# Kernel optimization log

Measured on AMD Instinct MI355X. Metric: run time of the kernel, lower is better.

## Reference

```python
import jax, jax.numpy as jnp
import numpy as np

B, C, H, W = 4, 96, 56, 56
K = 9          # kernel_size * dilation, dilation=1 so DenseDilated is identity
GROUPS = 4     # gcn_lib BasicConv uses groups=4 for the edge MLP 1x1 conv
EPS_BN = 1e-5
EPS_NORM = 1e-12


def _bn(x, p):
    # eval-mode BatchNorm2d: p = [gamma, beta, running_mean, running_var], each [C]
    g, b, m, v = p
    inv = g / jnp.sqrt(v + EPS_BN)
    sh = (1, -1) + (1,) * (x.ndim - 2)
    return x * inv.reshape(sh) + (b - m * inv).reshape(sh)


def _bn_params(k, c):
    k1, k2, k3, k4 = jax.random.split(k, 4)
    return jnp.stack([
        1.0 + 0.1 * jax.random.normal(k1, (c,)),
        0.1 * jax.random.normal(k2, (c,)),
        0.1 * jax.random.normal(k3, (c,)),
        jax.random.uniform(k4, (c,), minval=0.5, maxval=1.5),
    ])


def setup_inputs() -> dict:
    key = jax.random.key(0)
    ks = jax.random.split(key, 8)
    C2 = 2 * C
    return {
        "x": jax.random.normal(ks[0], (B, C, H, W), jnp.float32),
        "fc1_w": jax.random.normal(ks[1], (C, C), jnp.float32) / np.float32(np.sqrt(C)),
        "fc1_b": jnp.zeros((C,), jnp.float32),
        "bn1": _bn_params(ks[2], C),
        "gc_w": jax.random.normal(ks[3], (GROUPS, C2 // GROUPS, C2 // GROUPS), jnp.float32) / np.float32(np.sqrt(C2 // GROUPS)),
        "gc_b": jnp.zeros((C2,), jnp.float32),
        "bng": _bn_params(ks[4], C2),
        "fc2_w": jax.random.normal(ks[5], (C, C2), jnp.float32) / np.float32(np.sqrt(C2)),
        "fc2_b": jnp.zeros((C,), jnp.float32),
        "bn2": _bn_params(ks[6], C),
    }


def reference(x, fc1_w, fc1_b, bn1, gc_w, gc_b, bng, fc2_w, fc2_b, bn2):
    res = x
    # fc1: 1x1 conv + BN
    x = _bn(jnp.einsum('oc,bchw->bohw', fc1_w, x) + fc1_b[None, :, None, None], bn1)
    b, c, h, w = x.shape
    n = h * w
    xf = x.reshape(b, c, n)                       # [B,C,N] node features

    # --- dynamic kNN graph (torch.no_grad in original) ---
    xg = jax.lax.stop_gradient(xf)
    norm = jnp.sqrt(jnp.sum(xg * xg, axis=1, keepdims=True))
    xn = xg / jnp.maximum(norm, EPS_NORM)         # F.normalize along channels
    xt = xn.transpose(0, 2, 1)                    # [B,N,C]
    sq = jnp.sum(xt * xt, axis=-1)                # [B,N]
    neg_dist = 2.0 * jnp.einsum('bnc,bmc->bnm', xt, xt) - sq[:, :, None] - sq[:, None, :]
    _, nn_idx = jax.lax.top_k(neg_dist, K)        # [B,N,K] nearest neighbors

    # --- EdgeConv: gather, edge MLP (grouped 1x1 conv + BN + ReLU), max-aggregate ---
    x_j = jax.vmap(lambda f, idx: f[:, idx])(xf, nn_idx)   # [B,C,N,K]
    x_i = xf[:, :, :, None]                                 # [B,C,N,1]
    feat = jnp.concatenate([jnp.broadcast_to(x_i, x_j.shape), x_j - x_i], axis=1)  # [B,2C,N,K]
    c2 = 2 * c
    fg = feat.reshape(b, GROUPS, c2 // GROUPS, n, K)
    y = jnp.einsum('goc,bgcnk->bgonk', gc_w, fg).reshape(b, c2, n, K)
    y = y + gc_b[None, :, None, None]
    y = jax.nn.relu(_bn(y, bng))
    y = jnp.max(y, axis=-1)                       # max over K neighbors -> [B,2C,N]
    y = y.reshape(b, c2, h, w)

    # fc2: 1x1 conv + BN, residual
    y = _bn(jnp.einsum('oc,bchw->bohw', fc2_w, y) + fc2_b[None, :, None, None], bn2)
    return y + res
```

## Files before the change

kernel.cpp:

```cpp
#include <hip/hip_runtime.h>
#include <cstdint>
#include <cstddef>
#include <math.h>

#define BN_   4
#define CC    96
#define C2    192
#define NN    3136
#define KNN   9
#define TILE  64
#define PT    8
#define FJR   580
#define WTS   100

typedef __attribute__((ext_vector_type(8))) __bf16 bf16x8;
typedef __attribute__((ext_vector_type(4))) float f32x4;

__device__ __forceinline__ unsigned short f2bf(float f) {
  unsigned int u = __float_as_uint(f);
  unsigned int r = u + 0x7fffu + ((u >> 16) & 1u);
  return (unsigned short)(r >> 16);
}
__device__ __forceinline__ float bf2f(unsigned short h) {
  return __uint_as_float(((unsigned int)h) << 16);
}
__device__ __forceinline__ unsigned int fmono(float f) {
  unsigned int s = __float_as_uint(f);
  return s ^ ((unsigned int)((int)s >> 31) | 0x80000000u);
}

__device__ __forceinline__ void topk_ins(uint64_t key, uint64_t (&bk)[KNN]) {
  if (key > bk[KNN - 1]) {
    #pragma unroll
    for (int j = KNN - 1; j >= 1; --j) {
      bool aj   = bk[j]     > key;
      bool ajm1 = bk[j - 1] > key;
      bk[j] = aj ? bk[j] : (ajm1 ? key : bk[j - 1]);
    }
    bk[0] = (bk[0] > key) ? bk[0] : key;
  }
}

__global__ __launch_bounds__(256) void k_fc1(const float* __restrict__ x,
                                             const float* __restrict__ w,
                                             const float* __restrict__ bias,
                                             const float* __restrict__ bn,
                                             float* __restrict__ y1t,
                                             unsigned short* __restrict__ xh,
                                             unsigned short* __restrict__ xl,
                                             float* __restrict__ sq) {
  __shared__ float xs[CC * 64];
  __shared__ float wT[CC * WTS];
  __shared__ __align__(16) float ys[64 * CC];
  const int b = blockIdx.y, n0 = blockIdx.x * 64;
  const int t = threadIdx.x;
  for (int i = t; i < CC * 64; i += 256) {
    int c = i >> 6, nn = i & 63;
    xs[i] = x[((size_t)b * CC + c) * NN + n0 + nn];
  }
  for (int i = t; i < CC * CC; i += 256) {
    int o = i / CC, c = i % CC;
    wT[c * WTS + o] = w[i];
  }
  __syncthreads();
  const int nn = t & 63;
  const int og = __builtin_amdgcn_readfirstlane(t >> 6);
  float acc[24];
  #pragma unroll
  for (int i = 0; i < 24; ++i) acc[i] = 0.f;
  for (int c = 0; c < CC; ++c) {
    float xv = xs[c * 64 + nn];
    const float* wp = &wT[c * WTS + og * 24];
    float4 w0 = *(const float4*)(wp);
    float4 w1 = *(const float4*)(wp + 4);
    float4 w2 = *(const float4*)(wp + 8);
    float4 w3 = *(const float4*)(wp + 12);
    float4 w4 = *(const float4*)(wp + 16);
    float4 w5 = *(const float4*)(wp + 20);
    const float wv[24] = {w0.x, w0.y, w0.z, w0.w, w1.x, w1.y, w1.z, w1.w,
                          w2.x, w2.y, w2.z, w2.w, w3.x, w3.y, w3.z, w3.w,
                          w4.x, w4.y, w4.z, w4.w, w5.x, w5.y, w5.z, w5.w};
    #pragma unroll
    for (int oi = 0; oi < 24; ++oi) acc[oi] = fmaf(wv[oi], xv, acc[oi]);
  }
  #pragma unroll
  for (int oi = 0; oi < 24; ++oi) {
    int o = og * 24 + oi;
    float g = bn[o], be = bn[CC + o], mn = bn[2 * CC + o], vr = bn[3 * CC + o];
    float inv = g / sqrtf(vr + 1e-5f);
    float v = fmaf(acc[oi] + bias[o], inv, be - mn * inv);
    y1t[((size_t)b * NN + n0 + nn) * CC + o] = v;
    ys[nn * CC + o] = v;
  }
  __syncthreads();

  if (t < 64) {
    const size_t p = (size_t)b * NN + n0 + t;
    const float* row = &ys[t * CC];
    float s = 0.f;
    for (int c = 0; c < CC; c += 4) {
      float4 v = *(const float4*)(row + c);
      s += v.x * v.x; s += v.y * v.y; s += v.z * v.z; s += v.w * v.w;
    }
    float inv = 1.f / fmaxf(sqrtf(s), 1e-12f);
    float sqs = 0.f;
    unsigned short* hrow = xh + p * CC;
    unsigned short* lrow = xl + p * CC;
    for (int c = 0; c < CC; c += 4) {
      float4 v4 = *(const float4*)(row + c);
      float v0 = v4.x * inv, v1 = v4.y * inv, v2 = v4.z * inv, v3 = v4.w * inv;
      sqs += v0 * v0; sqs += v1 * v1; sqs += v2 * v2; sqs += v3 * v3;
      unsigned short h0 = f2bf(v0), h1 = f2bf(v1), h2 = f2bf(v2), h3 = f2bf(v3);
      float l0 = v0 - bf2f(h0), l1 = v1 - bf2f(h1), l2 = v2 - bf2f(h2), l3 = v3 - bf2f(h3);
      uint2 hv, lv;
      hv.x = (unsigned int)h0 | ((unsigned int)h1 << 16);
      hv.y = (unsigned int)h2 | ((unsigned int)h3 << 16);
      lv.x = (unsigned int)f2bf(l0) | ((unsigned int)f2bf(l1) << 16);
      lv.y = (unsigned int)f2bf(l2) | ((unsigned int)f2bf(l3) << 16);
      *(uint2*)&hrow[c] = hv;
      *(uint2*)&lrow[c] = lv;
    }
    sq[p] = sqs;
  }
}

__global__ __launch_bounds__(256) void k_dist(const unsigned short* __restrict__ xh,
                                              const unsigned short* __restrict__ xl,
                                              const float* __restrict__ sq,
                                              uint64_t* __restrict__ cand_k) {
  __shared__ __align__(16) unsigned short sB[2 * 64 * 104];
  __shared__ __align__(16) float sqm[TILE];
  unsigned short* BsH = sB;
  unsigned short* BsL = sB + 64 * 104;

  const int rt = blockIdx.x, chunk = blockIdx.y, b = blockIdx.z;
  const int nch = gridDim.y;
  const int r0 = rt * TILE;
  const int t = threadIdx.x;
  const int lane = t & 63, w = t >> 6;
  const int m16 = lane & 15, quad = lane >> 4;
  const int mt0 = (49 * chunk) / nch, mt1 = (49 * (chunk + 1)) / nch;

  const int gr = r0 + w * 16 + m16;
  bf16x8 ah[3], al[3];
  {
    const unsigned short* pH = xh + ((size_t)b * NN + gr) * CC + quad * 8;
    const unsigned short* pL = xl + ((size_t)b * NN + gr) * CC + quad * 8;
    #pragma unroll
    for (int kc = 0; kc < 3; ++kc) {
      ah[kc] = *(const bf16x8*)(pH + kc * 32);
      al[kc] = *(const bf16x8*)(pL + kc * 32);
    }
  }
  const float sr = sq[b * NN + gr];

  uint64_t bk[KNN];
  #pragma unroll
  for (int j = 0; j < KNN; ++j) bk[j] = 0ull;

  for (int mt = mt0; mt < mt1; ++mt) {
    const int m0 = mt * TILE;
    __syncthreads();
    for (int i = t; i < 64 * 12; i += 256) {
      int r = i / 12, ch = i % 12;
      const uint4* sH = (const uint4*)(xh + ((size_t)b * NN + m0 + r) * CC);
      const uint4* sL = (const uint4*)(xl + ((size_t)b * NN + m0 + r) * CC);
      *(uint4*)&BsH[r * 104 + ch * 8] = sH[ch];
      *(uint4*)&BsL[r * 104 + ch * 8] = sL[ch];
    }
    if (t < TILE) sqm[t] = sq[b * NN + m0 + t];
    __syncthreads();

    #pragma unroll
    for (int tt = 0; tt < 4; ++tt) {
      const int brow = (tt * 16 + m16) * 104 + quad * 8;
      f32x4 acc = {0.f, 0.f, 0.f, 0.f};
      #pragma unroll
      for (int kc = 0; kc < 3; ++kc) {
        bf16x8 bh = *(const bf16x8*)&BsH[brow + kc * 32];
        bf16x8 bl = *(const bf16x8*)&BsL[brow + kc * 32];
        acc = __builtin_amdgcn_mfma_f32_16x16x32_bf16(bh, ah[kc], acc, 0, 0, 0);
        acc = __builtin_amdgcn_mfma_f32_16x16x32_bf16(bl, ah[kc], acc, 0, 0, 0);
        acc = __builtin_amdgcn_mfma_f32_16x16x32_bf16(bh, al[kc], acc, 0, 0, 0);
      }
      float4 s4 = *(const float4*)&sqm[tt * 16 + quad * 4];
      const float sv[4] = {s4.x, s4.y, s4.z, s4.w};
      #pragma unroll
      for (int r = 0; r < 4; ++r) {
        float v = 2.f * acc[r] - sr - sv[r];
        int col = m0 + tt * 16 + quad * 4 + r;
        uint64_t key = ((uint64_t)fmono(v) << 32) | (unsigned int)~col;
        topk_ins(key, bk);
      }
    }
  }
  __syncthreads();

  uint64_t* sk = (uint64_t*)sB;
  #pragma unroll
  for (int j = 0; j < KNN; ++j) sk[((w * 16 + m16) * 4 + quad) * KNN + j] = bk[j];
  __syncthreads();
  if (t < TILE) {
    uint64_t fk[KNN];
    #pragma unroll
    for (int j = 0; j < KNN; ++j) fk[j] = 0ull;
    for (int qq = 0; qq < 4; ++qq)
      #pragma unroll
      for (int j = 0; j < KNN; ++j)
        topk_ins(sk[(t * 4 + qq) * KNN + j], fk);
    size_t base = (((size_t)b * nch + chunk) * NN + r0 + t) * KNN;
    #pragma unroll
    for (int j = 0; j < KNN; ++j) cand_k[base + j] = fk[j];
  }
}

__global__ __launch_bounds__(256) void k_nnmerge(const uint64_t* __restrict__ cand_k,
                                                 int* __restrict__ nn_idx, int nch) {
  __shared__ uint64_t sk[64 * 4 * KNN];
  const int t = threadIdx.x, lane = t & 63, sw = t >> 6;
  const int p = blockIdx.x * 64 + lane;
  const int b = p / NN, n = p % NN;
  const int cpw = nch >> 2;
  uint64_t fk[KNN];
  #pragma unroll
  for (int j = 0; j < KNN; ++j) fk[j] = 0ull;
  for (int ch = sw * cpw; ch < (sw + 1) * cpw; ++ch) {
    size_t base = (((size_t)b * nch + ch) * NN + n) * KNN;
    #pragma unroll
    for (int j = 0; j < KNN; ++j) topk_ins(cand_k[base + j], fk);
  }
  #pragma unroll
  for (int j = 0; j < KNN; ++j) sk[(lane * 4 + sw) * KNN + j] = fk[j];
  __syncthreads();
  if (sw == 0) {
    uint64_t gk[KNN];
    #pragma unroll
    for (int j = 0; j < KNN; ++j) gk[j] = 0ull;
    for (int q = 0; q < 4; ++q)
      #pragma unroll
      for (int j = 0; j < KNN; ++j)
        topk_ins(sk[(lane * 4 + q) * KNN + j], gk);
    #pragma unroll
    for (int j = 0; j < KNN; ++j) {
      int v = (int)(~(unsigned int)gk[j]);
      if ((unsigned)v >= (unsigned)NN) v = 0;
      nn_idx[(size_t)p * KNN + j] = v;
    }
  }
}

__global__ __launch_bounds__(256) void k_gconv(const float* __restrict__ y1t,
                                               const int* __restrict__ nn_idx,
                                               const float* __restrict__ gw,
                                               const float* __restrict__ gb,
                                               const float* __restrict__ bng,
                                               float* __restrict__ ymax) {
  __shared__ float wl[C2 * 49];
  __shared__ float xi[PT * CC];
  __shared__ __align__(16) float fj[PT * 2 * FJR];
  __shared__ int idxl[PT * KNN];
  const int t = threadIdx.x;
  const int p0 = blockIdx.x * PT;
  const int b0 = p0 / NN;

  for (int i = t; i < C2 * 48; i += 256) wl[(i / 48) * 49 + (i % 48)] = gw[i];
  if (t < PT * KNN) {
    int v = nn_idx[(size_t)p0 * KNN + t];
    idxl[t] = ((unsigned)v < (unsigned)NN) ? v : 0;
  }
  for (int i = t; i < PT * CC; i += 256) xi[i] = y1t[(size_t)p0 * CC + i];
  __syncthreads();

  for (int i = t; i < PT * KNN * CC; i += 256) {
    int pk = i / CC, c = i % CC;
    int p = pk / KNN, k = pk % KNN;
    int j = idxl[p * KNN + k];
    float v = y1t[((size_t)b0 * NN + j) * CC + c] - xi[p * CC + c];
    int h = (c >= 48) ? 1 : 0;
    fj[((p * 2 + h) * FJR) + (c - h * 48) * 12 + k] = v;
  }
  __syncthreads();

  const int p = t >> 5, l = t & 31;
  const size_t pg = p0 + p;
  float* orow = ymax + pg * C2;
  const float* xip = xi + p * CC;

  auto bnrelu = [&](int oc, float a) -> float {
    float g = bng[oc], be = bng[C2 + oc], mn = bng[2 * C2 + oc], vr = bng[3 * C2 + oc];
    float inv = g / sqrtf(vr + 1e-5f);
    return fmaxf(fmaf(a + gb[oc], inv, be - mn * inv), 0.f);
  };

  {
    const int oc0 = l, oc1 = l + 32, oc2 = l + 64;
    const int cb0 = (oc0 / 48) * 48, cb1 = (oc1 / 48) * 48, cb2 = (oc2 / 48) * 48;
    float a0 = 0.f, a1 = 0.f, a2 = 0.f;
    #pragma unroll 8
    for (int c = 0; c < 48; ++c) {
      a0 = fmaf(wl[oc0 * 49 + c], xip[cb0 + c], a0);
      a1 = fmaf(wl[oc1 * 49 + c], xip[cb1 + c], a1);
      a2 = fmaf(wl[oc2 * 49 + c], xip[cb2 + c], a2);
    }
    orow[oc0] = bnrelu(oc0, a0);
    orow[oc1] = bnrelu(oc1, a1);
    orow[oc2] = bnrelu(oc2, a2);
  }
  {
    const int half = l >> 4, lsub = l & 15;
    const int oc0 = 96 + half * 48 + lsub, oc1 = oc0 + 16, oc2 = oc0 + 32;
    const float* fbase = fj + ((size_t)p * 2 + half) * FJR;
    float acc0[KNN], acc1[KNN], acc2[KNN];
    #pragma unroll
    for (int k = 0; k < KNN; ++k) { acc0[k] = 0.f; acc1[k] = 0.f; acc2[k] = 0.f; }
    #pragma unroll 2
    for (int c = 0; c < 48; ++c) {
      float w0 = wl[oc0 * 49 + c], w1 = wl[oc1 * 49 + c], w2 = wl[oc2 * 49 + c];
      const float* fr = fbase + c * 12;
      float4 fA = *(const float4*)(fr);
      float4 fB = *(const float4*)(fr + 4);
      float f8 = fr[8];
      const float fk[KNN] = {fA.x, fA.y, fA.z, fA.w, fB.x, fB.y, fB.z, fB.w, f8};
      #pragma unroll
      for (int k = 0; k < KNN; ++k) {
        acc0[k] = fmaf(w0, fk[k], acc0[k]);
        acc1[k] = fmaf(w1, fk[k], acc1[k]);
        acc2[k] = fmaf(w2, fk[k], acc2[k]);
      }
    }
    {
      float g = bng[oc0], be = bng[C2 + oc0], mn = bng[2 * C2 + oc0], vr = bng[3 * C2 + oc0];
      float inv = g / sqrtf(vr + 1e-5f), sh = be - mn * inv, bs = gb[oc0], m = 0.f;
      #pragma unroll
      for (int k = 0; k < KNN; ++k) m = fmaxf(m, fmaxf(fmaf(acc0[k] + bs, inv, sh), 0.f));
      orow[oc0] = m;
    }
    {
      float g = bng[oc1], be = bng[C2 + oc1], mn = bng[2 * C2 + oc1], vr = bng[3 * C2 + oc1];
      float inv = g / sqrtf(vr + 1e-5f), sh = be - mn * inv, bs = gb[oc1], m = 0.f;
      #pragma unroll
      for (int k = 0; k < KNN; ++k) m = fmaxf(m, fmaxf(fmaf(acc1[k] + bs, inv, sh), 0.f));
      orow[oc1] = m;
    }
    {
      float g = bng[oc2], be = bng[C2 + oc2], mn = bng[2 * C2 + oc2], vr = bng[3 * C2 + oc2];
      float inv = g / sqrtf(vr + 1e-5f), sh = be - mn * inv, bs = gb[oc2], m = 0.f;
      #pragma unroll
      for (int k = 0; k < KNN; ++k) m = fmaxf(m, fmaxf(fmaf(acc2[k] + bs, inv, sh), 0.f));
      orow[oc2] = m;
    }
  }
}

__global__ __launch_bounds__(256) void k_fc2(const float* __restrict__ ymax,
                                             const float* __restrict__ w2,
                                             const float* __restrict__ b2,
                                             const float* __restrict__ bn2,
                                             const float* __restrict__ xin,
                                             float* __restrict__ out) {
  __shared__ float ys[64 * 193];
  __shared__ float w2T[C2 * WTS];
  const int b = blockIdx.y, n0 = blockIdx.x * 64, t = threadIdx.x;
  for (int i = t; i < 64 * C2; i += 256) {
    int nn = i / C2, c2 = i % C2;
    ys[nn * 193 + c2] = ymax[((size_t)b * NN + n0 + nn) * C2 + c2];
  }
  for (int i = t; i < CC * C2; i += 256) {
    int o = i / C2, c2 = i % C2;
    w2T[c2 * WTS + o] = w2[i];
  }
  __syncthreads();
  const int nn = t & 63;
  const int og = __builtin_amdgcn_readfirstlane(t >> 6);
  float acc[24];
  #pragma unroll
  for (int i = 0; i < 24; ++i) acc[i] = 0.f;
  const float* yrow = ys + nn * 193;
  for (int c2 = 0; c2 < C2; ++c2) {
    float yv = yrow[c2];
    const float* wp = &w2T[c2 * WTS + og * 24];
    float4 w0 = *(const float4*)(wp);
    float4 w1 = *(const float4*)(wp + 4);
    float4 w2v = *(const float4*)(wp + 8);
    float4 w3 = *(const float4*)(wp + 12);
    float4 w4 = *(const float4*)(wp + 16);
    float4 w5 = *(const float4*)(wp + 20);
    const float wv[24] = {w0.x, w0.y, w0.z, w0.w, w1.x, w1.y, w1.z, w1.w,
                          w2v.x, w2v.y, w2v.z, w2v.w, w3.x, w3.y, w3.z, w3.w,
                          w4.x, w4.y, w4.z, w4.w, w5.x, w5.y, w5.z, w5.w};
    #pragma unroll
    for (int oi = 0; oi < 24; ++oi) acc[oi] = fmaf(wv[oi], yv, acc[oi]);
  }
  #pragma unroll
  for (int oi = 0; oi < 24; ++oi) {
    int o = og * 24 + oi;
    float g = bn2[o], be = bn2[CC + o], mn = bn2[2 * CC + o], vr = bn2[3 * CC + o];
    float inv = g / sqrtf(vr + 1e-5f);
    float v = fmaf(acc[oi] + b2[o], inv, be - mn * inv);
    size_t off = ((size_t)b * CC + o) * NN + n0 + nn;
    out[off] = v + xin[off];
  }
}

extern "C" void kernel_launch(void* const* d_in, const int* in_sizes, int n_in,
                              void* d_out, int out_size, void* d_ws, size_t ws_size,
                              hipStream_t stream) {
  const float* x     = (const float*)d_in[0];
  const float* fc1_w = (const float*)d_in[1];
  const float* fc1_b = (const float*)d_in[2];
  const float* bn1   = (const float*)d_in[3];
  const float* gc_w  = (const float*)d_in[4];
  const float* gc_b  = (const float*)d_in[5];
  const float* bng   = (const float*)d_in[6];
  const float* fc2_w = (const float*)d_in[7];
  const float* fc2_b = (const float*)d_in[8];
  const float* bn2   = (const float*)d_in[9];
  float* out = (float*)d_out;

  const size_t BNC = (size_t)BN_ * NN * CC;
  float* ws = (float*)d_ws;
  float* y1t = ws;
  unsigned short* xh = (unsigned short*)(y1t + BNC);
  unsigned short* xl = xh + BNC;
  float* sq     = ws + 2 * BNC;
  float* ymax   = sq + (size_t)BN_ * NN;
  int* nnidx = (int*)(ymax + (size_t)BN_ * NN * C2);

  const size_t base_bytes =
      (2 * BNC + (size_t)BN_ * NN + (size_t)BN_ * NN * C2) * 4 +
      (size_t)BN_ * NN * KNN * 4;
  const size_t need16 = base_bytes + (size_t)BN_ * 16 * NN * KNN * 8;
  int nch;
  uint64_t* cand_k;
  if (ws_size >= need16) {
    nch = 16;
    cand_k = (uint64_t*)((char*)d_ws + base_bytes);
  } else {
    nch = 8;
    cand_k = (uint64_t*)ymax;
  }

  k_fc1<<<dim3(NN / 64, BN_), 256, 0, stream>>>(x, fc1_w, fc1_b, bn1, y1t, xh, xl, sq);
  k_dist<<<dim3(NN / TILE, nch, BN_), 256, 0, stream>>>(xh, xl, sq, cand_k);
  k_nnmerge<<<dim3((BN_ * NN) / 64), 256, 0, stream>>>(cand_k, nnidx, nch);
  k_gconv<<<dim3((BN_ * NN) / PT), 256, 0, stream>>>(y1t, nnidx, gc_w, gc_b, bng, ymax);
  k_fc2<<<dim3(NN / 64, BN_), 256, 0, stream>>>(ymax, fc2_w, fc2_b, bn2, x, out);
}
```

Baseline: 287.8 us.

## Precompute edge-conv linear map per node and gather projected features

Uses linearity of the grouped 1x1 conv: W*(x_j - x_i) = z_j - z_i, where z = W*x is computed once per node in the fc1 kernel. The x_i half of the edge MLP is also computed there and written straight to ymax. The gconv kernel becomes a light gather-subtract-BN-ReLU-max kernel, which removes the per-edge matmul work (about 9x redundant) and the large shared-memory staging. In exchange, fc1 does more compute and holds more shared memory, which may lower its occupancy. The workspace fallback logic also changes: candidates no longer alias ymax, and there is a 4-chunk fallback, since ymax is now written earlier.

```diff
diff --git a/kernel.cpp b/kernel.cpp
--- a/kernel.cpp
+++ b/kernel.cpp
@@ -10,8 +10,8 @@
 #define KNN   9
 #define TILE  64
 #define PT    8
-#define FJR   580
 #define WTS   100
+#define YSS   100
 
 typedef __attribute__((ext_vector_type(8))) __bf16 bf16x8;
 typedef __attribute__((ext_vector_type(4))) float f32x4;
@@ -45,13 +45,19 @@
                                              const float* __restrict__ w,
                                              const float* __restrict__ bias,
                                              const float* __restrict__ bn,
-                                             float* __restrict__ y1t,
+                                             const float* __restrict__ gcw,
+                                             const float* __restrict__ gcb,
+                                             const float* __restrict__ bng,
+                                             float* __restrict__ ymax,
+                                             float* __restrict__ zbuf,
                                              unsigned short* __restrict__ xh,
                                              unsigned short* __restrict__ xl,
                                              float* __restrict__ sq) {
   __shared__ float xs[CC * 64];
   __shared__ float wT[CC * WTS];
-  __shared__ __align__(16) float ys[64 * CC];
+  __shared__ __align__(16) float ys[64 * YSS];
+  __shared__ __align__(16) float gwl[C2 * 48];
+  __shared__ float bngL[5 * C2];
   const int b = blockIdx.y, n0 = blockIdx.x * 64;
   const int t = threadIdx.x;
   for (int i = t; i < CC * 64; i += 256) {
@@ -62,6 +68,9 @@
     int o = i / CC, c = i % CC;
     wT[c * WTS + o] = w[i];
   }
+  for (int i = t; i < C2 * 48; i += 256) gwl[i] = gcw[i];
+  for (int i = t; i < 4 * C2; i += 256) bngL[i] = bng[i];
+  if (t < C2) bngL[4 * C2 + t] = gcb[t];
   __syncthreads();
   const int nn = t & 63;
   const int og = __builtin_amdgcn_readfirstlane(t >> 6);
@@ -89,14 +98,48 @@
     float g = bn[o], be = bn[CC + o], mn = bn[2 * CC + o], vr = bn[3 * CC + o];
     float inv = g / sqrtf(vr + 1e-5f);
     float v = fmaf(acc[oi] + bias[o], inv, be - mn * inv);
-    y1t[((size_t)b * NN + n0 + nn) * CC + o] = v;
-    ys[nn * CC + o] = v;
-  }
-  __syncthreads();
+    ys[nn * YSS + o] = v;
+  }
+  __syncthreads();
+
+  {
+    const int cb = (og & 1) * 48;
+    const float* yrow = &ys[nn * YSS + cb];
+    float xv[48];
+    #pragma unroll
+    for (int c4 = 0; c4 < 12; ++c4) {
+      float4 v4 = *(const float4*)(yrow + c4 * 4);
+      xv[c4 * 4 + 0] = v4.x; xv[c4 * 4 + 1] = v4.y;
+      xv[c4 * 4 + 2] = v4.z; xv[c4 * 4 + 3] = v4.w;
+    }
+    const size_t pg = (size_t)b * NN + n0 + nn;
+    if (og < 2) {
+      for (int oi = 0; oi < 48; ++oi) {
+        int oc = og * 48 + oi;
+        const float* wr = &gwl[oc * 48];
+        float a = 0.f;
+        #pragma unroll 8
+        for (int c = 0; c < 48; ++c) a = fmaf(wr[c], xv[c], a);
+        float g = bngL[oc], be = bngL[C2 + oc], mn = bngL[2 * C2 + oc],
+              vr = bngL[3 * C2 + oc], bs = bngL[4 * C2 + oc];
+        float inv = g / sqrtf(vr + 1e-5f);
+        ymax[pg * C2 + oc] = fmaxf(fmaf(a + bs, inv, be - mn * inv), 0.f);
+      }
+    } else {
+      for (int oi = 0; oi < 48; ++oi) {
+        int zoc = (og - 2) * 48 + oi;
+        const float* wr = &gwl[(96 + zoc) * 48];
+        float a = 0.f;
+        #pragma unroll 8
+        for (int c = 0; c < 48; ++c) a = fmaf(wr[c], xv[c], a);
+        zbuf[pg * CC + zoc] = a;
+      }
+    }
+  }
 
   if (t < 64) {
     const size_t p = (size_t)b * NN + n0 + t;
-    const float* row = &ys[t * CC];
+    const float* row = &ys[t * YSS];
     float s = 0.f;
     for (int c = 0; c < CC; c += 4) {
       float4 v = *(const float4*)(row + c);
@@ -249,107 +292,46 @@
   }
 }
 
-__global__ __launch_bounds__(256) void k_gconv(const float* __restrict__ y1t,
-                                               const int* __restrict__ nn_idx,
-                                               const float* __restrict__ gw,
-                                               const float* __restrict__ gb,
-                                               const float* __restrict__ bng,
-                                               float* __restrict__ ymax) {
-  __shared__ float wl[C2 * 49];
-  __shared__ float xi[PT * CC];
-  __shared__ __align__(16) float fj[PT * 2 * FJR];
+__global__ __launch_bounds__(256) void k_gmax(const float* __restrict__ zbuf,
+                                              const int* __restrict__ nn_idx,
+                                              const float* __restrict__ gb,
+                                              const float* __restrict__ bng,
+                                              float* __restrict__ ymax) {
   __shared__ int idxl[PT * KNN];
   const int t = threadIdx.x;
   const int p0 = blockIdx.x * PT;
   const int b0 = p0 / NN;
-
-  for (int i = t; i < C2 * 48; i += 256) wl[(i / 48) * 49 + (i % 48)] = gw[i];
   if (t < PT * KNN) {
     int v = nn_idx[(size_t)p0 * KNN + t];
     idxl[t] = ((unsigned)v < (unsigned)NN) ? v : 0;
   }
-  for (int i = t; i < PT * CC; i += 256) xi[i] = y1t[(size_t)p0 * CC + i];
-  __syncthreads();
-
-  for (int i = t; i < PT * KNN * CC; i += 256) {
-    int pk = i / CC, c = i % CC;
-    int p = pk / KNN, k = pk % KNN;
-    int j = idxl[p * KNN + k];
-    float v = y1t[((size_t)b0 * NN + j) * CC + c] - xi[p * CC + c];
-    int h = (c >= 48) ? 1 : 0;
-    fj[((p * 2 + h) * FJR) + (c - h * 48) * 12 + k] = v;
-  }
-  __syncthreads();
-
+  __syncthreads();
   const int p = t >> 5, l = t & 31;
   const size_t pg = p0 + p;
-  float* orow = ymax + pg * C2;
-  const float* xip = xi + p * CC;
-
-  auto bnrelu = [&](int oc, float a) -> float {
-    float g = bng[oc], be = bng[C2 + oc], mn = bng[2 * C2 + oc], vr = bng[3 * C2 + oc];
-    float inv = g / sqrtf(vr + 1e-5f);
-    return fmaxf(fmaf(a + gb[oc], inv, be - mn * inv), 0.f);
-  };
-
-  {
-    const int oc0 = l, oc1 = l + 32, oc2 = l + 64;
-    const int cb0 = (oc0 / 48) * 48, cb1 = (oc1 / 48) * 48, cb2 = (oc2 / 48) * 48;
-    float a0 = 0.f, a1 = 0.f, a2 = 0.f;
-    #pragma unroll 8
-    for (int c = 0; c < 48; ++c) {
-      a0 = fmaf(wl[oc0 * 49 + c], xip[cb0 + c], a0);
-      a1 = fmaf(wl[oc1 * 49 + c], xip[cb1 + c], a1);
-      a2 = fmaf(wl[oc2 * 49 + c], xip[cb2 + c], a2);
-    }
-    orow[oc0] = bnrelu(oc0, a0);
-    orow[oc1] = bnrelu(oc1, a1);
-    orow[oc2] = bnrelu(oc2, a2);
-  }
-  {
-    const int half = l >> 4, lsub = l & 15;
-    const int oc0 = 96 + half * 48 + lsub, oc1 = oc0 + 16, oc2 = oc0 + 32;
-    const float* fbase = fj + ((size_t)p * 2 + half) * FJR;
-    float acc0[KNN], acc1[KNN], acc2[KNN];
-    #pragma unroll
-    for (int k = 0; k < KNN; ++k) { acc0[k] = 0.f; acc1[k] = 0.f; acc2[k] = 0.f; }
-    #pragma unroll 2
-    for (int c = 0; c < 48; ++c) {
-      float w0 = wl[oc0 * 49 + c], w1 = wl[oc1 * 49 + c], w2 = wl[oc2 * 49 + c];
-      const float* fr = fbase + c * 12;
-      float4 fA = *(const float4*)(fr);
-      float4 fB = *(const float4*)(fr + 4);
-      float f8 = fr[8];
-      const float fk[KNN] = {fA.x, fA.y, fA.z, fA.w, fB.x, fB.y, fB.z, fB.w, f8};
-      #pragma unroll
-      for (int k = 0; k < KNN; ++k) {
-        acc0[k] = fmaf(w0, fk[k], acc0[k]);
-        acc1[k] = fmaf(w1, fk[k], acc1[k]);
-        acc2[k] = fmaf(w2, fk[k], acc2[k]);
-      }
-    }
-    {
-      float g = bng[oc0], be = bng[C2 + oc0], mn = bng[2 * C2 + oc0], vr = bng[3 * C2 + oc0];
-      float inv = g / sqrtf(vr + 1e-5f), sh = be - mn * inv, bs = gb[oc0], m = 0.f;
-      #pragma unroll
-      for (int k = 0; k < KNN; ++k) m = fmaxf(m, fmaxf(fmaf(acc0[k] + bs, inv, sh), 0.f));
-      orow[oc0] = m;
-    }
-    {
-      float g = bng[oc1], be = bng[C2 + oc1], mn = bng[2 * C2 + oc1], vr = bng[3 * C2 + oc1];
-      float inv = g / sqrtf(vr + 1e-5f), sh = be - mn * inv, bs = gb[oc1], m = 0.f;
-      #pragma unroll
-      for (int k = 0; k < KNN; ++k) m = fmaxf(m, fmaxf(fmaf(acc1[k] + bs, inv, sh), 0.f));
-      orow[oc1] = m;
-    }
-    {
-      float g = bng[oc2], be = bng[C2 + oc2], mn = bng[2 * C2 + oc2], vr = bng[3 * C2 + oc2];
-      float inv = g / sqrtf(vr + 1e-5f), sh = be - mn * inv, bs = gb[oc2], m = 0.f;
-      #pragma unroll
-      for (int k = 0; k < KNN; ++k) m = fmaxf(m, fmaxf(fmaf(acc2[k] + bs, inv, sh), 0.f));
-      orow[oc2] = m;
-    }
-  }
+  const float* zi = zbuf + pg * CC;
+  const float* zb = zbuf + (size_t)b0 * NN * CC;
+  const float zi0 = zi[l], zi1 = zi[l + 32], zi2 = zi[l + 64];
+  const int o0 = 96 + l, o1 = o0 + 32, o2 = o0 + 64;
+  const float inv0 = bng[o0] / sqrtf(bng[3 * C2 + o0] + 1e-5f);
+  const float inv1 = bng[o1] / sqrtf(bng[3 * C2 + o1] + 1e-5f);
+  const float inv2 = bng[o2] / sqrtf(bng[3 * C2 + o2] + 1e-5f);
+  const float sh0 = bng[C2 + o0] - bng[2 * C2 + o0] * inv0;
+  const float sh1 = bng[C2 + o1] - bng[2 * C2 + o1] * inv1;
+  const float sh2 = bng[C2 + o2] - bng[2 * C2 + o2] * inv2;
+  const float bs0 = gb[o0], bs1 = gb[o1], bs2 = gb[o2];
+  float m0 = 0.f, m1 = 0.f, m2 = 0.f;
+  #pragma unroll
+  for (int k = 0; k < KNN; ++k) {
+    const float* zj = zb + (size_t)idxl[p * KNN + k] * CC;
+    float a0 = zj[l]      - zi0;
+    float a1 = zj[l + 32] - zi1;
+    float a2 = zj[l + 64] - zi2;
+    m0 = fmaxf(m0, fmaxf(fmaf(a0 + bs0, inv0, sh0), 0.f));
+    m1 = fmaxf(m1, fmaxf(fmaf(a1 + bs1, inv1, sh1), 0.f));
+    m2 = fmaxf(m2, fmaxf(fmaf(a2 + bs2, inv2, sh2), 0.f));
+  }
+  float* orow = ymax + pg * C2 + 96;
+  orow[l] = m0; orow[l + 32] = m1; orow[l + 64] = m2;
 }
 
 __global__ __launch_bounds__(256) void k_fc2(const float* __restrict__ ymax,
@@ -419,8 +401,8 @@
 
   const size_t BNC = (size_t)BN_ * NN * CC;
   float* ws = (float*)d_ws;
-  float* y1t = ws;
-  unsigned short* xh = (unsigned short*)(y1t + BNC);
+  float* zbuf = ws;
+  unsigned short* xh = (unsigned short*)(zbuf + BNC);
   unsigned short* xl = xh + BNC;
   float* sq     = ws + 2 * BNC;
   float* ymax   = sq + (size_t)BN_ * NN;
@@ -429,20 +411,16 @@
   const size_t base_bytes =
       (2 * BNC + (size_t)BN_ * NN + (size_t)BN_ * NN * C2) * 4 +
       (size_t)BN_ * NN * KNN * 4;
-  const size_t need16 = base_bytes + (size_t)BN_ * 16 * NN * KNN * 8;
+  uint64_t* cand_k = (uint64_t*)((char*)d_ws + base_bytes);
   int nch;
-  uint64_t* cand_k;
-  if (ws_size >= need16) {
-    nch = 16;
-    cand_k = (uint64_t*)((char*)d_ws + base_bytes);
-  } else {
-    nch = 8;
-    cand_k = (uint64_t*)ymax;
-  }
-
-  k_fc1<<<dim3(NN / 64, BN_), 256, 0, stream>>>(x, fc1_w, fc1_b, bn1, y1t, xh, xl, sq);
+  if (ws_size >= base_bytes + (size_t)BN_ * 16 * NN * KNN * 8)      nch = 16;
+  else if (ws_size >= base_bytes + (size_t)BN_ * 8 * NN * KNN * 8)  nch = 8;
+  else                                                              nch = 4;
+
+  k_fc1<<<dim3(NN / 64, BN_), 256, 0, stream>>>(x, fc1_w, fc1_b, bn1, gc_w,
+                                                gc_b, bng, ymax, zbuf, xh, xl, sq);
   k_dist<<<dim3(NN / TILE, nch, BN_), 256, 0, stream>>>(xh, xl, sq, cand_k);
   k_nnmerge<<<dim3((BN_ * NN) / 64), 256, 0, stream>>>(cand_k, nnidx, nch);
-  k_gconv<<<dim3((BN_ * NN) / PT), 256, 0, stream>>>(y1t, nnidx, gc_w, gc_b, bng, ymax);
+  k_gmax<<<dim3((BN_ * NN) / PT), 256, 0, stream>>>(zbuf, nnidx, gc_b, bng, ymax);
   k_fc2<<<dim3(NN / 64, BN_), 256, 0, stream>>>(ymax, fc2_w, fc2_b, bn2, x, out);
 }
```

Result: slower. 317.4 us (+10.3%).
